# Optimization experiments

Measured on AMD Instinct MI355X. Metric: run time of the kernel, lower is better.

The kernel has to match this reference:

```python
import jax, jax.numpy as jnp
import numpy as np

N_HEAD = 16
ROPE_THETA = 10000.0


def _rope_cache(T, dim, theta=ROPE_THETA):
    # inv_freq over even indices, as in RotaryEmbedding
    inv_freq = 1.0 / (theta ** (jnp.arange(0, dim, 2, dtype=jnp.float32) / dim))
    freqs = jnp.arange(T, dtype=jnp.float32)[:, None] * inv_freq[None, :]  # [T, dim//2]
    return jnp.cos(freqs), jnp.sin(freqs)


def _apply_rope(x, cos, sin):
    # x: [B, H, T, D]; cos/sin: [T, D//2] broadcast over B,H
    x1 = x[..., ::2]
    x2 = x[..., 1::2]
    # even slots: x1*cos - x2*sin ; odd slots: x2*cos + x1*sin (interleaved rotate-pairs)
    r1 = x1 * cos - x2 * sin
    r2 = x2 * cos + x1 * sin
    return jnp.stack([r1, r2], axis=-1).reshape(x.shape)


def setup_inputs() -> dict:
    key = jax.random.key(0)
    k1, k2, k3 = jax.random.split(key, 3)
    B, T, C = 4, 2048, 1024
    x = jax.random.normal(k1, (B, T, C), dtype=jnp.float32)
    W_qkv = jax.random.normal(k2, (C, 3 * C), dtype=jnp.float32) * (C ** -0.5)
    W_out = jax.random.normal(k3, (C, C), dtype=jnp.float32) * (C ** -0.5)
    return {"x": x, "W_qkv": W_qkv, "W_out": W_out}


def reference(x, W_qkv, W_out):
    B, T, C = x.shape
    H = N_HEAD
    D = C // H
    # fused QKV projection -> [3, B, H, T, D]
    qkv = (x @ W_qkv).reshape(B, T, 3, H, D).transpose(2, 0, 3, 1, 4)
    q, k, v = qkv[0], qkv[1], qkv[2]
    cos, sin = _rope_cache(T, D)
    q = _apply_rope(q, cos, sin)
    k = _apply_rope(k, cos, sin)
    scale = 1.0 / jnp.sqrt(jnp.float32(D))
    scores = jnp.einsum('bhqd,bhkd->bhqk', q, k) * scale  # [B,H,T,T]
    causal_mask = jnp.tril(jnp.ones((T, T), dtype=bool))
    scores = jnp.where(causal_mask, scores, -jnp.inf)
    attn = jax.nn.softmax(scores, axis=-1)
    out = jnp.einsum('bhqk,bhkd->bhqd', attn, v)  # [B,H,T,D]
    out = out.transpose(0, 2, 1, 3).reshape(B, T, C)
    return out @ W_out
```

## Files before the change

kernel.cpp:

```cpp
#include <hip/hip_runtime.h>
#include <hip/hip_bf16.h>
#include <math.h>

#define BATCH 4
#define SEQ   2048
#define CDIM  1024
#define NHEAD 16
#define HDIM  64
#define QKVN  3072
#define QSCALE 0.1803368801111244f

typedef float f32x4 __attribute__((ext_vector_type(4)));
typedef float f32x16 __attribute__((ext_vector_type(16)));
typedef short bf16x8 __attribute__((ext_vector_type(8)));
typedef short bf16x4 __attribute__((ext_vector_type(4)));
typedef int i32x2 __attribute__((ext_vector_type(2)));
typedef int i32x4 __attribute__((ext_vector_type(4)));

static __device__ __forceinline__ unsigned short f2bf(float f) {
    unsigned int u = __float_as_uint(f);
    u += 0x7FFF + ((u >> 16) & 1);
    return (unsigned short)(u >> 16);
}
static __device__ __forceinline__ float bf2f(unsigned short u) {
    return __uint_as_float(((unsigned int)u) << 16);
}
static __device__ __forceinline__ unsigned int pk2bf(float lo, float hi) {
    __hip_bfloat162 h = __float22bfloat162_rn(make_float2(lo, hi));
    return *(unsigned int*)&h;
}
static __device__ __forceinline__ bf16x8 lds_read8(const unsigned short* p) {
    bf16x4 lo = *(const bf16x4*)p;
    bf16x4 hi = *(const bf16x4*)(p + 4);
    return __builtin_shufflevector(lo, hi, 0, 1, 2, 3, 4, 5, 6, 7);
}

__global__ __launch_bounds__(256) void build_ctab(float2* __restrict__ ctab) {
    const int i = blockIdx.x * 256 + threadIdx.x;
    const int dp = i & 31;
    const int t = i >> 5;
    const float invf = powf(10000.0f, -((float)(2 * dp)) / 64.0f);
    float sv, cv;
    __sincosf((float)t * invf, &sv, &cv);
    ctab[i] = make_float2(cv, sv);
}

__global__ __launch_bounds__(256) void convert_bf16(const float* __restrict__ src,
                                                    unsigned short* __restrict__ dst,
                                                    int n4) {
    int i = blockIdx.x * 256 + threadIdx.x;
    if (i >= n4) return;
    float4 v = ((const float4*)src)[i];
    ushort4 o;
    o.x = f2bf(v.x); o.y = f2bf(v.y); o.z = f2bf(v.z); o.w = f2bf(v.w);
    ((ushort4*)dst)[i] = o;
}

__global__ __launch_bounds__(256) void transpose_bf16(const float* __restrict__ W,
                                                      unsigned short* __restrict__ Wt,
                                                      int K, int N) {
    __shared__ unsigned short tile[64][65];
    const int tid = threadIdx.x;
    const int n0 = blockIdx.x * 64;
    const int k0 = blockIdx.y * 64;
    const int r = tid >> 4;
    const int c4 = (tid & 15) << 2;
    #pragma unroll
    for (int ii = 0; ii < 4; ii++) {
        int row = r + 16 * ii;
        float4 v = *(const float4*)&W[(size_t)(k0 + row) * N + n0 + c4];
        tile[c4 + 0][row] = f2bf(v.x);
        tile[c4 + 1][row] = f2bf(v.y);
        tile[c4 + 2][row] = f2bf(v.z);
        tile[c4 + 3][row] = f2bf(v.w);
    }
    __syncthreads();
    #pragma unroll
    for (int ii = 0; ii < 4; ii++) {
        int row = r + 16 * ii;
        ushort4 o;
        o.x = tile[row][c4 + 0];
        o.y = tile[row][c4 + 1];
        o.z = tile[row][c4 + 2];
        o.w = tile[row][c4 + 3];
        *(ushort4*)&Wt[(size_t)(n0 + row) * K + k0 + c4] = o;
    }
}

#define GLDS(gp, lp) __builtin_amdgcn_global_load_lds(                       \
    (const __attribute__((address_space(1))) unsigned int*)(gp),             \
    (__attribute__((address_space(3))) unsigned int*)(lp), 16, 0, 0)

template <typename OUT>
__global__ __launch_bounds__(256) void gemm_bt_bf16(
    const unsigned short* __restrict__ A,
    const unsigned short* __restrict__ Bt,
    OUT* __restrict__ C, int M, int N, int K) {
    __shared__ unsigned short As[128 * 32];
    __shared__ unsigned short Bs[128 * 32];

    const int tid = threadIdx.x;
    const int wave = tid >> 6;
    const int lane = tid & 63;
    const int bm = blockIdx.y * 128;
    const int bn = blockIdx.x * 128;
    const int wm = (wave >> 1) * 64;
    const int wn = (wave & 1) * 64;

    const int srow = tid >> 2;
    const int scol = (((tid & 3) ^ ((tid >> 3) & 3)) << 3);
    const unsigned short* Ag0 = A + (size_t)(bm + srow) * K + scol;
    const unsigned short* Ag1 = A + (size_t)(bm + 64 + srow) * K + scol;
    const unsigned short* Bg0 = Bt + (size_t)(bn + srow) * K + scol;
    const unsigned short* Bg1 = Bt + (size_t)(bn + 64 + srow) * K + scol;
    char* AsW = (char*)As + wave * 1024;
    char* BsW = (char*)Bs + wave * 1024;

    const int fm = lane & 15;
    const int quad = lane >> 4;
    const int ck = (quad ^ ((fm >> 1) & 3)) << 3;

    f32x4 acc[4][4];
    #pragma unroll
    for (int i = 0; i < 4; i++)
        #pragma unroll
        for (int j = 0; j < 4; j++)
            acc[i][j] = (f32x4){0.f, 0.f, 0.f, 0.f};

    for (int k0 = 0; k0 < K; k0 += 32) {
        GLDS(Ag0 + k0, AsW);
        GLDS(Ag1 + k0, AsW + 4096);
        GLDS(Bg0 + k0, BsW);
        GLDS(Bg1 + k0, BsW + 4096);
        __syncthreads();

        bf16x8 af[4], bfr[4];
        #pragma unroll
        for (int i = 0; i < 4; i++)
            af[i] = *(const bf16x8*)&As[(wm + i * 16 + fm) * 32 + ck];
        #pragma unroll
        for (int j = 0; j < 4; j++)
            bfr[j] = *(const bf16x8*)&Bs[(wn + j * 16 + fm) * 32 + ck];
        #pragma unroll
        for (int i = 0; i < 4; i++)
            #pragma unroll
            for (int j = 0; j < 4; j++)
                acc[i][j] = __builtin_amdgcn_mfma_f32_16x16x32_bf16(
                    af[i], bfr[j], acc[i][j], 0, 0, 0);
        __syncthreads();
    }

    const int er = quad * 4;
    #pragma unroll
    for (int i = 0; i < 4; i++) {
        #pragma unroll
        for (int j = 0; j < 4; j++) {
            #pragma unroll
            for (int r = 0; r < 4; r++) {
                size_t off = (size_t)(bm + wm + i * 16 + er + r) * N + bn + wn + j * 16 + fm;
                if constexpr (sizeof(OUT) == 2)
                    C[off] = f2bf(acc[i][j][r]);
                else
                    C[off] = acc[i][j][r];
            }
        }
    }
}

__global__ __launch_bounds__(256) void gemm_qkv_fused(
    const unsigned short* __restrict__ A,
    const unsigned short* __restrict__ Bt,
    const float2* __restrict__ ctab,
    unsigned short* __restrict__ Qg,
    unsigned short* __restrict__ Kg,
    unsigned short* __restrict__ Vtg) {
    __shared__ unsigned short SH[8448];
    unsigned short* As = SH;
    unsigned short* Bs = SH + 4096;
    const int K = CDIM;

    const int tid = threadIdx.x;
    const int wave = tid >> 6;
    const int lane = tid & 63;
    const int bm = blockIdx.y * 128;
    const int bn = blockIdx.x * 128;
    const int wm = (wave >> 1) * 64;
    const int wn = (wave & 1) * 64;

    const int srow = tid >> 2;
    const int scol = (((tid & 3) ^ ((tid >> 3) & 3)) << 3);
    const unsigned short* Ag0 = A + (size_t)(bm + srow) * K + scol;
    const unsigned short* Ag1 = A + (size_t)(bm + 64 + srow) * K + scol;
    const unsigned short* Bg0 = Bt + (size_t)(bn + srow) * K + scol;
    const unsigned short* Bg1 = Bt + (size_t)(bn + 64 + srow) * K + scol;
    char* AsW = (char*)SH + wave * 1024;
    char* BsW = (char*)SH + 8192 + wave * 1024;

    const int fm = lane & 15;
    const int quad = lane >> 4;
    const int ck = (quad ^ ((fm >> 1) & 3)) << 3;

    f32x4 acc[4][4];
    #pragma unroll
    for (int i = 0; i < 4; i++)
        #pragma unroll
        for (int j = 0; j < 4; j++)
            acc[i][j] = (f32x4){0.f, 0.f, 0.f, 0.f};

    for (int k0 = 0; k0 < K; k0 += 32) {
        GLDS(Ag0 + k0, AsW);
        GLDS(Ag1 + k0, AsW + 4096);
        GLDS(Bg0 + k0, BsW);
        GLDS(Bg1 + k0, BsW + 4096);
        __syncthreads();

        bf16x8 af[4], bfr[4];
        #pragma unroll
        for (int i = 0; i < 4; i++)
            af[i] = *(const bf16x8*)&As[(wm + i * 16 + fm) * 32 + ck];
        #pragma unroll
        for (int j = 0; j < 4; j++)
            bfr[j] = *(const bf16x8*)&Bs[(wn + j * 16 + fm) * 32 + ck];
        #pragma unroll
        for (int i = 0; i < 4; i++)
            #pragma unroll
            for (int j = 0; j < 4; j++)
                acc[i][j] = __builtin_amdgcn_mfma_f32_16x16x32_bf16(
                    af[i], bfr[j], acc[i][j], 0, 0, 0);
        __syncthreads();
    }

    const int s = bn >> 10;
    const int hbase = (bn & 1023) >> 6;
    const int b = bm >> 11;
    const int t0 = bm & 2047;

    #pragma unroll 1
    for (int pass = 0; pass < 2; pass++) {
        if ((wave >> 1) == pass) {
            #pragma unroll
            for (int i = 0; i < 4; i++)
                #pragma unroll
                for (int j = 0; j < 4; j++)
                    #pragma unroll
                    for (int r = 0; r < 4; r++)
                        SH[(i * 16 + quad * 4 + r) * 132 + wn + j * 16 + fm] =
                            f2bf(acc[i][j][r]);
        }
        __syncthreads();

        if (s < 2) {
            unsigned short* dst = (s == 0) ? Qg : Kg;
            const float sc = (s == 0) ? QSCALE : 1.0f;
            #pragma unroll
            for (int it = 0; it < 16; it++) {
                const int idx = it * 256 + tid;
                const int row = idx >> 6;
                const int col = (idx & 63) << 1;
                const unsigned int pr = *(const unsigned int*)&SH[row * 132 + col];
                const float x0 = bf2f((unsigned short)pr);
                const float x1 = bf2f((unsigned short)(pr >> 16));
                const int t = t0 + pass * 64 + row;
                const int h = hbase + (col >> 6);
                const int d = col & 63;
                const float2 cs = ctab[t * 32 + (d >> 1)];
                const float r0 = (x0 * cs.x - x1 * cs.y) * sc;
                const float r1 = (x1 * cs.x + x0 * cs.y) * sc;
                *(unsigned int*)&dst[((size_t)(b * NHEAD + h) * SEQ + t) * HDIM + d] =
                    pk2bf(r0, r1);
            }
        } else {
            #pragma unroll
            for (int it = 0; it < 8; it++) {
                const int idx = it * 256 + tid;
                const int dcol = idx >> 4;
                const int tq = idx & 15;
                ushort4 o;
                o.x = SH[(tq * 4 + 0) * 132 + dcol];
                o.y = SH[(tq * 4 + 1) * 132 + dcol];
                o.z = SH[(tq * 4 + 2) * 132 + dcol];
                o.w = SH[(tq * 4 + 3) * 132 + dcol];
                const int h = hbase + (dcol >> 6);
                const int dl = dcol & 63;
                const int t = t0 + pass * 64 + tq * 4;
                *(ushort4*)&Vtg[((size_t)(b * NHEAD + h) * HDIM + dl) * SEQ + t] = o;
            }
        }
        __syncthreads();
    }
}

__global__ __launch_bounds__(256, 4) void flash_attn_mfma(
    const unsigned short* __restrict__ Qg,
    const unsigned short* __restrict__ Kg,
    const unsigned short* __restrict__ Vtg,
    unsigned short* __restrict__ att) {
    __shared__ unsigned short Ks[2][64 * 68];
    __shared__ unsigned short Vt[2][64 * 68];

    const int tid = threadIdx.x;
    const int wave = tid >> 6;
    const int lane = tid & 63;
    const int l31 = lane & 31;
    const int hi = lane >> 5;
    const int wq = wave * 32;
    const int bh = blockIdx.x & 63;
    const int qt = 15 - (blockIdx.x >> 6);
    const int b = bh >> 4, h = bh & 15;

    const int r_ld = tid >> 4;
    const int c4 = (tid & 15) << 2;

    const unsigned short* Kbase = Kg + (size_t)bh * SEQ * HDIM;
    const unsigned short* Vbase = Vtg + (size_t)bh * HDIM * SEQ;

    const int qrow = qt * 128 + wq + l31;

    bf16x8 bq[4];
    #pragma unroll
    for (int dc = 0; dc < 4; dc++)
        bq[dc] = *(const bf16x8*)&Qg[((size_t)bh * SEQ + qrow) * HDIM + dc * 16 + hi * 8];

    f32x16 O[2];
    #pragma unroll
    for (int nt = 0; nt < 2; nt++)
        #pragma unroll
        for (int r = 0; r < 16; r++) O[nt][r] = 0.f;
    float lsum = 0.f;

    const int jtop = 2 * qt + 1;

    ushort4 kreg[4], vreg[4];
    #pragma unroll
    for (int ii = 0; ii < 4; ii++) {
        const int row = r_ld + 16 * ii;
        kreg[ii] = *(const ushort4*)&Kbase[(size_t)row * HDIM + c4];
        vreg[ii] = *(const ushort4*)&Vbase[(size_t)row * SEQ + c4];
    }
    #pragma unroll
    for (int ii = 0; ii < 4; ii++) {
        const int row = r_ld + 16 * ii;
        *(ushort4*)&Ks[0][row * 68 + c4] = kreg[ii];
        *(ushort4*)&Vt[0][row * 68 + c4] = vreg[ii];
    }
    __syncthreads();

    int cur = 0;
    #pragma unroll 1
    for (int j = 0; j <= jtop; j++) {
        if (j < jtop) {
            #pragma unroll
            for (int ii = 0; ii < 4; ii++) {
                const int row = r_ld + 16 * ii;
                kreg[ii] = *(const ushort4*)&Kbase[(size_t)((j + 1) * 64 + row) * HDIM + c4];
                vreg[ii] = *(const ushort4*)&Vbase[(size_t)row * SEQ + (j + 1) * 64 + c4];
            }
        }

        const bool active = (j * 64) <= (qt * 128 + wq + 31);
        if (active) {
            const unsigned short* Kc = Ks[cur];
            const unsigned short* Vc = Vt[cur];
            const bool diag = (j * 64 + 63) > (qt * 128 + wq);

            #pragma unroll
            for (int kt = 0; kt < 2; kt++) {
                f32x16 sa;
                #pragma unroll
                for (int r = 0; r < 16; r++) sa[r] = 0.f;
                __builtin_amdgcn_s_setprio(1);
                #pragma unroll
                for (int dc = 0; dc < 4; dc++) {
                    bf16x8 ak = lds_read8(&Kc[(kt * 32 + l31) * 68 + dc * 16 + hi * 8]);
                    sa = __builtin_amdgcn_mfma_f32_32x32x16_bf16(ak, bq[dc], sa, 0, 0, 0);
                }
                __builtin_amdgcn_s_setprio(0);

                if (diag) {
                    const int kb = j * 64 + kt * 32 + 4 * hi;
                    #pragma unroll
                    for (int r = 0; r < 16; r++) {
                        const int kg = kb + (r & 3) + 8 * (r >> 2);
                        if (kg > qrow) sa[r] = -INFINITY;
                    }
                }

                float e[16];
                #pragma unroll
                for (int r = 0; r < 16; r++) {
                    e[r] = exp2f(sa[r]);
                    lsum += e[r];
                }
                unsigned int p32[8];
                #pragma unroll
                for (int v = 0; v < 8; v++)
                    p32[v] = pk2bf(e[2 * v], e[2 * v + 1]);

                #pragma unroll
                for (int c = 0; c < 2; c++) {
                    i32x2 s0 = __builtin_amdgcn_permlane32_swap(
                        (int)p32[4 * c + 0], (int)p32[4 * c + 2], false, false);
                    i32x2 s1 = __builtin_amdgcn_permlane32_swap(
                        (int)p32[4 * c + 1], (int)p32[4 * c + 3], false, false);
                    i32x4 pw = (i32x4){s0[0], s1[0], s0[1], s1[1]};
                    bf16x8 pa = *(bf16x8*)&pw;
                    __builtin_amdgcn_s_setprio(1);
                    #pragma unroll
                    for (int nt = 0; nt < 2; nt++) {
                        bf16x8 bv = lds_read8(&Vc[(nt * 32 + l31) * 68 + kt * 32 + c * 16 + hi * 8]);
                        O[nt] = __builtin_amdgcn_mfma_f32_32x32x16_bf16(pa, bv, O[nt], 0, 0, 0);
                    }
                    __builtin_amdgcn_s_setprio(0);
                }
            }
        }

        if (j < jtop) {
            const int nb = cur ^ 1;
            #pragma unroll
            for (int ii = 0; ii < 4; ii++) {
                const int row = r_ld + 16 * ii;
                *(ushort4*)&Ks[nb][row * 68 + c4] = kreg[ii];
                *(ushort4*)&Vt[nb][row * 68 + c4] = vreg[ii];
            }
        }

        __syncthreads();
        cur ^= 1;
    }

    const float lfull = lsum + __shfl_xor(lsum, 32);
    const float inv = 1.0f / lfull;
    #pragma unroll
    for (int r = 0; r < 16; r++) {
        const int qloc = (r & 3) + 8 * (r >> 2) + 4 * hi;
        const float invr = __uint_as_float((unsigned int)__builtin_amdgcn_ds_bpermute(
            qloc * 4, (int)__float_as_uint(inv)));
        const int row = qt * 128 + wq + qloc;
        #pragma unroll
        for (int nt = 0; nt < 2; nt++)
            att[(size_t)(b * SEQ + row) * CDIM + h * HDIM + nt * 32 + l31] =
                f2bf(O[nt][r] * invr);
    }
}

extern "C" void kernel_launch(void* const* d_in, const int* in_sizes, int n_in,
                              void* d_out, int out_size, void* d_ws, size_t ws_size,
                              hipStream_t stream) {
    const float* x     = (const float*)d_in[0];
    const float* W_qkv = (const float*)d_in[1];
    const float* W_out = (const float*)d_in[2];
    float* out = (float*)d_out;

    const int M = BATCH * SEQ;

    float2* ctab = (float2*)d_ws;
    unsigned short* xb   = (unsigned short*)(ctab + SEQ * 32);
    unsigned short* wqb  = xb + (size_t)M * CDIM;
    unsigned short* wob  = wqb + (size_t)CDIM * QKVN;
    unsigned short* attb = wob + (size_t)CDIM * CDIM;
    unsigned short* Qg   = attb + (size_t)M * CDIM;
    unsigned short* Kg   = Qg + (size_t)M * CDIM;
    unsigned short* Vtg  = Kg + (size_t)M * CDIM;

    build_ctab<<<(SEQ * 32) / 256, 256, 0, stream>>>(ctab);
    convert_bf16<<<(M * CDIM / 4 + 255) / 256, 256, 0, stream>>>(x, xb, M * CDIM / 4);
    transpose_bf16<<<dim3(QKVN / 64, CDIM / 64), 256, 0, stream>>>(W_qkv, wqb, CDIM, QKVN);
    transpose_bf16<<<dim3(CDIM / 64, CDIM / 64), 256, 0, stream>>>(W_out, wob, CDIM, CDIM);

    gemm_qkv_fused<<<dim3(QKVN / 128, M / 128), 256, 0, stream>>>(
        xb, wqb, ctab, Qg, Kg, Vtg);

    flash_attn_mfma<<<BATCH * NHEAD * (SEQ / 128), 256, 0, stream>>>(Qg, Kg, Vtg, attb);

    gemm_bt_bf16<float><<<dim3(CDIM / 128, M / 128), 256, 0, stream>>>(
        attb, wob, out, M, CDIM, CDIM);
}
```

Baseline: 270.6 us.

## Merge prep kernels, double-buffer GEMM LDS loads, and swizzle block order

Merges the four preprocessing launches (x conversion, RoPE table, two weight transposes) into one kernel that branches on block index. Both GEMMs now double-buffer their LDS tiles, so the next K-slice is prefetched while the current one feeds MFMA, and one barrier per iteration is dropped. A block-index swizzle remaps workgroups to improve L2 reuse. This doubles LDS use per block, which may lower occupancy, and the QKV epilogue reuses the same shared buffer after a final barrier.

```diff
diff --git a/kernel.cpp b/kernel.cpp
--- a/kernel.cpp
+++ b/kernel.cpp
@@ -35,34 +35,11 @@
     return __builtin_shufflevector(lo, hi, 0, 1, 2, 3, 4, 5, 6, 7);
 }
 
-__global__ __launch_bounds__(256) void build_ctab(float2* __restrict__ ctab) {
-    const int i = blockIdx.x * 256 + threadIdx.x;
-    const int dp = i & 31;
-    const int t = i >> 5;
-    const float invf = powf(10000.0f, -((float)(2 * dp)) / 64.0f);
-    float sv, cv;
-    __sincosf((float)t * invf, &sv, &cv);
-    ctab[i] = make_float2(cv, sv);
-}
-
-__global__ __launch_bounds__(256) void convert_bf16(const float* __restrict__ src,
-                                                    unsigned short* __restrict__ dst,
-                                                    int n4) {
-    int i = blockIdx.x * 256 + threadIdx.x;
-    if (i >= n4) return;
-    float4 v = ((const float4*)src)[i];
-    ushort4 o;
-    o.x = f2bf(v.x); o.y = f2bf(v.y); o.z = f2bf(v.z); o.w = f2bf(v.w);
-    ((ushort4*)dst)[i] = o;
-}
-
-__global__ __launch_bounds__(256) void transpose_bf16(const float* __restrict__ W,
-                                                      unsigned short* __restrict__ Wt,
-                                                      int K, int N) {
-    __shared__ unsigned short tile[64][65];
-    const int tid = threadIdx.x;
-    const int n0 = blockIdx.x * 64;
-    const int k0 = blockIdx.y * 64;
+static __device__ __forceinline__ void transpose_tile(
+    const float* __restrict__ W, unsigned short* __restrict__ Wt,
+    int K, int N, int bx, int by, unsigned short (*tile)[65], int tid) {
+    const int n0 = bx * 64;
+    const int k0 = by * 64;
     const int r = tid >> 4;
     const int c4 = (tid & 15) << 2;
     #pragma unroll
@@ -87,6 +64,37 @@
     }
 }
 
+__global__ __launch_bounds__(256) void prep(
+    const float* __restrict__ x, const float* __restrict__ W_qkv,
+    const float* __restrict__ W_out, float2* __restrict__ ctab,
+    unsigned short* __restrict__ xb, unsigned short* __restrict__ wqb,
+    unsigned short* __restrict__ wob) {
+    __shared__ unsigned short tile[64][65];
+    const int blk = blockIdx.x;
+    const int tid = threadIdx.x;
+    if (blk < 8192) {
+        const int i = blk * 256 + tid;
+        float4 v = ((const float4*)x)[i];
+        ushort4 o;
+        o.x = f2bf(v.x); o.y = f2bf(v.y); o.z = f2bf(v.z); o.w = f2bf(v.w);
+        ((ushort4*)xb)[i] = o;
+    } else if (blk < 8448) {
+        const int i = (blk - 8192) * 256 + tid;
+        const int dp = i & 31;
+        const int t = i >> 5;
+        const float invf = powf(10000.0f, -((float)(2 * dp)) / 64.0f);
+        float sv, cv;
+        __sincosf((float)t * invf, &sv, &cv);
+        ctab[i] = make_float2(cv, sv);
+    } else if (blk < 9216) {
+        const int r = blk - 8448;
+        transpose_tile(W_qkv, wqb, CDIM, QKVN, r % 48, r / 48, tile, tid);
+    } else {
+        const int r = blk - 9216;
+        transpose_tile(W_out, wob, CDIM, CDIM, r % 16, r / 16, tile, tid);
+    }
+}
+
 #define GLDS(gp, lp) __builtin_amdgcn_global_load_lds(                       \
     (const __attribute__((address_space(1))) unsigned int*)(gp),             \
     (__attribute__((address_space(3))) unsigned int*)(lp), 16, 0, 0)
@@ -96,14 +104,19 @@
     const unsigned short* __restrict__ A,
     const unsigned short* __restrict__ Bt,
     OUT* __restrict__ C, int M, int N, int K) {
-    __shared__ unsigned short As[128 * 32];
-    __shared__ unsigned short Bs[128 * 32];
+    __shared__ unsigned short As[2][128 * 32];
+    __shared__ unsigned short Bs[2][128 * 32];
 
     const int tid = threadIdx.x;
     const int wave = tid >> 6;
     const int lane = tid & 63;
-    const int bm = blockIdx.y * 128;
-    const int bn = blockIdx.x * 128;
+
+    const int nwg = gridDim.x * gridDim.y;
+    const int flat = blockIdx.y * gridDim.x + blockIdx.x;
+    const int swz = (flat & 7) * (nwg >> 3) + (flat >> 3);
+    const int bn = (swz % gridDim.x) * 128;
+    const int bm = (swz / gridDim.x) * 128;
+
     const int wm = (wave >> 1) * 64;
     const int wn = (wave & 1) * 64;
 
@@ -113,8 +126,6 @@
     const unsigned short* Ag1 = A + (size_t)(bm + 64 + srow) * K + scol;
     const unsigned short* Bg0 = Bt + (size_t)(bn + srow) * K + scol;
     const unsigned short* Bg1 = Bt + (size_t)(bn + 64 + srow) * K + scol;
-    char* AsW = (char*)As + wave * 1024;
-    char* BsW = (char*)Bs + wave * 1024;
 
     const int fm = lane & 15;
     const int quad = lane >> 4;
@@ -127,27 +138,39 @@
         for (int j = 0; j < 4; j++)
             acc[i][j] = (f32x4){0.f, 0.f, 0.f, 0.f};
 
+    {
+        char* AsW = (char*)As[0] + wave * 1024;
+        char* BsW = (char*)Bs[0] + wave * 1024;
+        GLDS(Ag0, AsW); GLDS(Ag1, AsW + 4096);
+        GLDS(Bg0, BsW); GLDS(Bg1, BsW + 4096);
+    }
+
+    int cur = 0;
     for (int k0 = 0; k0 < K; k0 += 32) {
-        GLDS(Ag0 + k0, AsW);
-        GLDS(Ag1 + k0, AsW + 4096);
-        GLDS(Bg0 + k0, BsW);
-        GLDS(Bg1 + k0, BsW + 4096);
         __syncthreads();
-
+        if (k0 + 32 < K) {
+            char* AsW = (char*)As[cur ^ 1] + wave * 1024;
+            char* BsW = (char*)Bs[cur ^ 1] + wave * 1024;
+            GLDS(Ag0 + k0 + 32, AsW); GLDS(Ag1 + k0 + 32, AsW + 4096);
+            GLDS(Bg0 + k0 + 32, BsW); GLDS(Bg1 + k0 + 32, BsW + 4096);
+        }
+
+        const unsigned short* Ar = As[cur];
+        const unsigned short* Br = Bs[cur];
         bf16x8 af[4], bfr[4];
         #pragma unroll
         for (int i = 0; i < 4; i++)
-            af[i] = *(const bf16x8*)&As[(wm + i * 16 + fm) * 32 + ck];
+            af[i] = *(const bf16x8*)&Ar[(wm + i * 16 + fm) * 32 + ck];
         #pragma unroll
         for (int j = 0; j < 4; j++)
-            bfr[j] = *(const bf16x8*)&Bs[(wn + j * 16 + fm) * 32 + ck];
+            bfr[j] = *(const bf16x8*)&Br[(wn + j * 16 + fm) * 32 + ck];
         #pragma unroll
         for (int i = 0; i < 4; i++)
             #pragma unroll
             for (int j = 0; j < 4; j++)
                 acc[i][j] = __builtin_amdgcn_mfma_f32_16x16x32_bf16(
                     af[i], bfr[j], acc[i][j], 0, 0, 0);
-        __syncthreads();
+        cur ^= 1;
     }
 
     const int er = quad * 4;
@@ -174,16 +197,19 @@
     unsigned short* __restrict__ Qg,
     unsigned short* __restrict__ Kg,
     unsigned short* __restrict__ Vtg) {
-    __shared__ unsigned short SH[8448];
-    unsigned short* As = SH;
-    unsigned short* Bs = SH + 4096;
+    __shared__ unsigned short SH[16384];
     const int K = CDIM;
 
     const int tid = threadIdx.x;
     const int wave = tid >> 6;
     const int lane = tid & 63;
-    const int bm = blockIdx.y * 128;
-    const int bn = blockIdx.x * 128;
+
+    const int nwg = gridDim.x * gridDim.y;
+    const int flat = blockIdx.y * gridDim.x + blockIdx.x;
+    const int swz = (flat & 7) * (nwg >> 3) + (flat >> 3);
+    const int bn = (swz % gridDim.x) * 128;
+    const int bm = (swz / gridDim.x) * 128;
+
     const int wm = (wave >> 1) * 64;
     const int wn = (wave & 1) * 64;
 
@@ -193,8 +219,6 @@
     const unsigned short* Ag1 = A + (size_t)(bm + 64 + srow) * K + scol;
     const unsigned short* Bg0 = Bt + (size_t)(bn + srow) * K + scol;
     const unsigned short* Bg1 = Bt + (size_t)(bn + 64 + srow) * K + scol;
-    char* AsW = (char*)SH + wave * 1024;
-    char* BsW = (char*)SH + 8192 + wave * 1024;
 
     const int fm = lane & 15;
     const int quad = lane >> 4;
@@ -207,28 +231,42 @@
         for (int j = 0; j < 4; j++)
             acc[i][j] = (f32x4){0.f, 0.f, 0.f, 0.f};
 
+    {
+        char* AsW = (char*)SH + wave * 1024;
+        char* BsW = (char*)SH + 8192 + wave * 1024;
+        GLDS(Ag0, AsW); GLDS(Ag1, AsW + 4096);
+        GLDS(Bg0, BsW); GLDS(Bg1, BsW + 4096);
+    }
+
+    int cur = 0;
     for (int k0 = 0; k0 < K; k0 += 32) {
-        GLDS(Ag0 + k0, AsW);
-        GLDS(Ag1 + k0, AsW + 4096);
-        GLDS(Bg0 + k0, BsW);
-        GLDS(Bg1 + k0, BsW + 4096);
         __syncthreads();
-
+        if (k0 + 32 < K) {
+            const int nb = (cur ^ 1) * 16384;
+            char* AsW = (char*)SH + nb + wave * 1024;
+            char* BsW = (char*)SH + nb + 8192 + wave * 1024;
+            GLDS(Ag0 + k0 + 32, AsW); GLDS(Ag1 + k0 + 32, AsW + 4096);
+            GLDS(Bg0 + k0 + 32, BsW); GLDS(Bg1 + k0 + 32, BsW + 4096);
+        }
+
+        const unsigned short* Ar = SH + cur * 8192;
+        const unsigned short* Br = Ar + 4096;
         bf16x8 af[4], bfr[4];
         #pragma unroll
         for (int i = 0; i < 4; i++)
-            af[i] = *(const bf16x8*)&As[(wm + i * 16 + fm) * 32 + ck];
+            af[i] = *(const bf16x8*)&Ar[(wm + i * 16 + fm) * 32 + ck];
         #pragma unroll
         for (int j = 0; j < 4; j++)
-            bfr[j] = *(const bf16x8*)&Bs[(wn + j * 16 + fm) * 32 + ck];
+            bfr[j] = *(const bf16x8*)&Br[(wn + j * 16 + fm) * 32 + ck];
         #pragma unroll
         for (int i = 0; i < 4; i++)
             #pragma unroll
             for (int j = 0; j < 4; j++)
                 acc[i][j] = __builtin_amdgcn_mfma_f32_16x16x32_bf16(
                     af[i], bfr[j], acc[i][j], 0, 0, 0);
-        __syncthreads();
-    }
+        cur ^= 1;
+    }
+    __syncthreads();
 
     const int s = bn >> 10;
     const int hbase = (bn & 1023) >> 6;
@@ -463,10 +501,7 @@
     unsigned short* Kg   = Qg + (size_t)M * CDIM;
     unsigned short* Vtg  = Kg + (size_t)M * CDIM;
 
-    build_ctab<<<(SEQ * 32) / 256, 256, 0, stream>>>(ctab);
-    convert_bf16<<<(M * CDIM / 4 + 255) / 256, 256, 0, stream>>>(x, xb, M * CDIM / 4);
-    transpose_bf16<<<dim3(QKVN / 64, CDIM / 64), 256, 0, stream>>>(W_qkv, wqb, CDIM, QKVN);
-    transpose_bf16<<<dim3(CDIM / 64, CDIM / 64), 256, 0, stream>>>(W_out, wob, CDIM, CDIM);
+    prep<<<9472, 256, 0, stream>>>(x, W_qkv, W_out, ctab, xb, wqb, wob);
 
     gemm_qkv_fused<<<dim3(QKVN / 128, M / 128), 256, 0, stream>>>(
         xb, wqb, ctab, Qg, Kg, Vtg);
```

Measured after the change: 280.9 us. 3.8% more time.
